# Optimization experiments

Hardware: AMD Instinct MI355X
Metric: run time of the kernel (lower is better)

Reference implementation:

```python
import jax, jax.numpy as jnp
import numpy as np
from jax import lax

BS, NT, CH, K = 8, 128, 1024, 4
H = 512  # num_output_chanls // 2 per direction (bidirectional)
G = 4 * H  # gate dim, PyTorch order i,f,g,o


def setup_inputs() -> dict:
    key = jax.random.key(0)
    ks = jax.random.split(key, 9)
    s = 1.0 / np.sqrt(H)
    u = lambda k_, shape: jax.random.uniform(k_, shape, jnp.float32, -s, s)
    return {
        "inputs": jax.random.normal(ks[0], (BS, NT, CH, K), jnp.float32),
        "Wih_f": u(ks[1], (K, G, CH)),
        "Whh_f": u(ks[2], (K, G, H)),
        "bih_f": u(ks[3], (K, G)),
        "bhh_f": u(ks[4], (K, G)),
        "Wih_b": u(ks[5], (K, G, CH)),
        "Whh_b": u(ks[6], (K, G, H)),
        "bih_b": u(ks[7], (K, G)),
        "bhh_b": u(ks[8], (K, G)),
    }


def _lstm_dir(x_tbck, Wih, Whh, bih, bhh, reverse):
    # x_tbck: [nt, bs, ch, k]; weights batched over k heads.
    bs = x_tbck.shape[1]
    k, _, h = Whh.shape
    bias = bih + bhh  # [k, 4h]

    def step(carry, x_t):
        h_prev, c_prev = carry
        # detach_hidden_state=True: hidden state detached each step
        h_prev = lax.stop_gradient(h_prev)
        c_prev = lax.stop_gradient(c_prev)
        gates = (jnp.einsum('bck,kgc->bkg', x_t, Wih)
                 + jnp.einsum('bkh,kgh->bkg', h_prev, Whh)
                 + bias)  # [bs, k, 4h]
        i, f, g, o = jnp.split(gates, 4, axis=-1)
        c_new = jax.nn.sigmoid(f) * c_prev + jax.nn.sigmoid(i) * jnp.tanh(g)
        h_new = jax.nn.sigmoid(o) * jnp.tanh(c_new)
        return (h_new, c_new), h_new

    init = (jnp.zeros((bs, k, h), x_tbck.dtype), jnp.zeros((bs, k, h), x_tbck.dtype))
    _, hs = lax.scan(step, init, x_tbck, reverse=reverse)  # [nt, bs, k, h]
    return hs


def reference(inputs, Wih_f, Whh_f, bih_f, bhh_f, Wih_b, Whh_b, bih_b, bhh_b):
    # inputs: [bs, nt, ch, k] -> scan over time
    x = jnp.transpose(inputs, (1, 0, 2, 3))  # [nt, bs, ch, k]
    hs_f = _lstm_dir(x, Wih_f, Whh_f, bih_f, bhh_f, reverse=False)
    hs_b = _lstm_dir(x, Wih_b, Whh_b, bih_b, bhh_b, reverse=True)
    # [nt, bs, k, h] -> [bs, nt, h, k]; concat forward/backward on hidden dim
    hs_f = jnp.transpose(hs_f, (1, 0, 3, 2))
    hs_b = jnp.transpose(hs_b, (1, 0, 3, 2))
    return jnp.concatenate([hs_f, hs_b], axis=2)  # [bs, nt, 2h, k]
```

## Files before the change

kernel.cpp:

```cpp
#include <hip/hip_runtime.h>
#include <stdint.h>


typedef __attribute__((ext_vector_type(8))) short short8;
typedef __attribute__((ext_vector_type(4))) float floatx4;
typedef unsigned long long ull;

#define POISON 0x7FC07FC07FC07FC0ull

#define GLOAD_LDS16(g, l)                                        \
  __builtin_amdgcn_global_load_lds(                              \
      (const __attribute__((address_space(1))) void*)(g),        \
      (__attribute__((address_space(3))) void*)(l), 16, 0, 0)

__device__ __forceinline__ unsigned short f2bf(float f) {
  unsigned u = __float_as_uint(f);
  u = (u + 0x7fffu + ((u >> 16) & 1u)) >> 16;
  return (unsigned short)u;
}
__device__ __forceinline__ float sigm(float x) { return 1.0f / (1.0f + __expf(-x)); }
__device__ __forceinline__ float tanh_f(float x) {
  float ax = fabsf(x);
  float e = __expf(-2.0f * ax);
  float t = (1.0f - e) / (1.0f + e);
  return x < 0.0f ? -t : t;
}

__global__ void pack_x_k(const float* __restrict__ x, unsigned short* __restrict__ Xp) {
  int g = blockIdx.x * 256 + threadIdx.x;
  int m = g >> 10, c = g & 1023;
  int t = m >> 3, b = m & 7;
  float4 v = *(const float4*)(x + ((size_t)((b * 128 + t) * 1024 + c)) * 4);
  Xp[g]           = f2bf(v.x);
  Xp[1048576 + g] = f2bf(v.y);
  Xp[2097152 + g] = f2bf(v.z);
  Xp[3145728 + g] = f2bf(v.w);
}

__global__ void cast_bf_k(const float* __restrict__ src, unsigned short* __restrict__ dst, int n4) {
  int i = blockIdx.x * 256 + threadIdx.x;
  if (i >= n4) return;
  float4 v = ((const float4*)src)[i];
  ushort4 o;
  o.x = f2bf(v.x); o.y = f2bf(v.y); o.z = f2bf(v.z); o.w = f2bf(v.w);
  ((ushort4*)dst)[i] = o;
}

__global__ void bias_k(const float* __restrict__ bihf, const float* __restrict__ bhhf,
                       const float* __restrict__ bihb, const float* __restrict__ bhhb,
                       float* __restrict__ bias) {
  int i = blockIdx.x * 256 + threadIdx.x;
  int dk = i >> 11, g = i & 2047, kk = dk & 3;
  const float* a = (dk < 4) ? bihf : bihb;
  const float* b = (dk < 4) ? bhhf : bhhb;
  bias[i] = a[kk * 2048 + g] + b[kk * 2048 + g];
}

__global__ void fill_poison_k(ull* __restrict__ p) {
  p[(size_t)blockIdx.x * 256 + threadIdx.x] = POISON;
}

__global__ __launch_bounds__(256) void gemm_ih_k(
    const unsigned short* __restrict__ Xp, const unsigned short* __restrict__ Wb,
    const float* __restrict__ bias, float* __restrict__ ih) {
  const int mt = blockIdx.x, ntl = blockIdx.y, dk = blockIdx.z;
  const int kh = dk & 3;
  const int tid = threadIdx.x;
  const int L = tid & 63, w = tid >> 6;
  const int wm = w & 1, wn = w >> 1;
  const int quad = L >> 4, lo = L & 15;

  __shared__ unsigned short As[128 * 32];
  __shared__ unsigned short Bs[128 * 32];

  const unsigned short* Ab = Xp + (size_t)kh * 1048576 + (size_t)mt * 128 * 1024;
  const unsigned short* Bb = Wb + (size_t)dk * 2097152 + (size_t)ntl * 128 * 1024;

  floatx4 acc[4][4] = {};

  for (int kc = 0; kc < 32; ++kc) {
#pragma unroll
    for (int q = 0; q < 2; ++q) {
      int c = q * 256 + w * 64 + L;
      int ldsb = (q * 256 + w * 64) * 8;
      GLOAD_LDS16(Ab + (size_t)(c >> 2) * 1024 + kc * 32 + (c & 3) * 8, As + ldsb);
      GLOAD_LDS16(Bb + (size_t)(c >> 2) * 1024 + kc * 32 + (c & 3) * 8, Bs + ldsb);
    }
    __syncthreads();
    short8 af[4], bf[4];
#pragma unroll
    for (int mi = 0; mi < 4; ++mi)
      af[mi] = *(const short8*)(As + (wm * 64 + mi * 16 + lo) * 32 + quad * 8);
#pragma unroll
    for (int ni = 0; ni < 4; ++ni)
      bf[ni] = *(const short8*)(Bs + (wn * 64 + ni * 16 + lo) * 32 + quad * 8);
#pragma unroll
    for (int mi = 0; mi < 4; ++mi)
#pragma unroll
      for (int ni = 0; ni < 4; ++ni)
        acc[mi][ni] = __builtin_amdgcn_mfma_f32_16x16x32_bf16(af[mi], bf[ni], acc[mi][ni], 0, 0, 0);
    __syncthreads();
  }

#pragma unroll
  for (int mi = 0; mi < 4; ++mi)
#pragma unroll
    for (int ni = 0; ni < 4; ++ni) {
      int g = ntl * 128 + wn * 64 + ni * 16 + lo;
      float bv = bias[dk * 2048 + g];
#pragma unroll
      for (int r = 0; r < 4; ++r) {
        int m = mt * 128 + wm * 64 + mi * 16 + quad * 4 + r;
        ih[((size_t)dk * 1024 + m) * 2048 + g] = acc[mi][ni][r] + bv;
      }
    }
}

__global__ __launch_bounds__(256) void lstm_rec_k(
    const float* __restrict__ ih, const unsigned short* __restrict__ whh,
    float* __restrict__ out, ull* __restrict__ stateS) {
  const int tid = threadIdx.x;
  const int L = tid & 63;
  const int w = tid >> 6;
  const int grp = blockIdx.x & 7;
  const int d = grp >> 2, kh = grp & 3;
  const int wg = blockIdx.x >> 3;
  const int j0 = wg * 32;
  const int quad = L >> 4, lo = L & 15;

  __shared__ unsigned short h_lds[16 * 520];
  __shared__ float gbuf[4][8][32];

  for (int i = tid; i < 16 * 520; i += 256) h_lds[i] = 0;

  short8 bfrag[2][16];
#pragma unroll
  for (int ni = 0; ni < 2; ++ni) {
    const unsigned short* wb =
        whh + ((size_t)grp * 2048 + (size_t)(w * 512 + j0 + ni * 16 + lo)) * 512 + quad * 8;
#pragma unroll
    for (int kk = 0; kk < 16; ++kk) bfrag[ni][kk] = *(const short8*)(wb + kk * 32);
  }

  const int pb = tid >> 5, pjj = tid & 31;
  float creg = 0.0f;

  float ihv[2][4];
  {
    int t0 = d ? 127 : 0;
#pragma unroll
    for (int ni = 0; ni < 2; ++ni) {
      const float* ihp =
          ih + ((size_t)grp * 1024 + (size_t)t0 * 8) * 2048 + (w * 512 + j0 + ni * 16 + lo);
#pragma unroll
      for (int r = 0; r < 4; ++r) {
        int b = quad * 4 + r;
        ihv[ni][r] = (b < 8) ? ihp[(size_t)b * 2048] : 0.0f;
      }
    }
  }

  const int srow = tid >> 5;
  const int scol = (tid & 31) * 16;

  for (int s = 0; s < 128; ++s) {
    const int t = d ? (127 - s) : s;

    if (s) {
      const ull* src = stateS + ((size_t)grp * 128 + s) * 1024 + tid * 4;
      ull v0, v1, v2, v3;
      do {
        v0 = __hip_atomic_load(src + 0, __ATOMIC_RELAXED, __HIP_MEMORY_SCOPE_AGENT);
        v1 = __hip_atomic_load(src + 1, __ATOMIC_RELAXED, __HIP_MEMORY_SCOPE_AGENT);
        v2 = __hip_atomic_load(src + 2, __ATOMIC_RELAXED, __HIP_MEMORY_SCOPE_AGENT);
        v3 = __hip_atomic_load(src + 3, __ATOMIC_RELAXED, __HIP_MEMORY_SCOPE_AGENT);
      } while (v0 == POISON || v1 == POISON || v2 == POISON || v3 == POISON);
      unsigned short* dl = h_lds + srow * 520 + scol;
      *(ull*)(dl + 0) = v0;
      *(ull*)(dl + 4) = v1;
      *(ull*)(dl + 8) = v2;
      *(ull*)(dl + 12) = v3;
    }
    __syncthreads();

    floatx4 acc[2] = {};
    {
      const unsigned short* ar = h_lds + lo * 520 + quad * 8;
#pragma unroll
      for (int kk = 0; kk < 16; ++kk) {
        short8 a = *(const short8*)(ar + kk * 32);
#pragma unroll
        for (int ni = 0; ni < 2; ++ni)
          acc[ni] = __builtin_amdgcn_mfma_f32_16x16x32_bf16(a, bfrag[ni][kk], acc[ni], 0, 0, 0);
      }
    }
#pragma unroll
    for (int ni = 0; ni < 2; ++ni)
#pragma unroll
      for (int r = 0; r < 4; ++r) {
        int b = quad * 4 + r;
        if (b < 8) gbuf[w][b][ni * 16 + lo] = acc[ni][r] + ihv[ni][r];
      }

    if (s < 127) {
      int tn = d ? (126 - s) : (s + 1);
#pragma unroll
      for (int ni = 0; ni < 2; ++ni) {
        const float* ihp =
            ih + ((size_t)grp * 1024 + (size_t)tn * 8) * 2048 + (w * 512 + j0 + ni * 16 + lo);
#pragma unroll
        for (int r = 0; r < 4; ++r) {
          int b = quad * 4 + r;
          ihv[ni][r] = (b < 8) ? ihp[(size_t)b * 2048] : 0.0f;
        }
      }
    }
    __syncthreads();

    {
      float ig = gbuf[0][pb][pjj], fg = gbuf[1][pb][pjj];
      float gg = gbuf[2][pb][pjj], og = gbuf[3][pb][pjj];
      float cn = sigm(fg) * creg + sigm(ig) * tanh_f(gg);
      creg = cn;
      float h = sigm(og) * tanh_f(cn);

      if (s < 127) {
        unsigned hs = f2bf(h);
        int base = L & ~3;
        unsigned v0 = __shfl(hs, base + 0);
        unsigned v1 = __shfl(hs, base + 1);
        unsigned v2 = __shfl(hs, base + 2);
        unsigned v3 = __shfl(hs, base + 3);
        if ((L & 3) == 0) {
          ull wv = (ull)v0 | ((ull)v1 << 16) | ((ull)v2 << 32) | ((ull)v3 << 48);
          ull* dst = stateS + ((size_t)grp * 128 + (s + 1)) * 1024 + pb * 128 + ((j0 + pjj) >> 2);
          __hip_atomic_store(dst, wv, __ATOMIC_RELAXED, __HIP_MEMORY_SCOPE_AGENT);
        }
      }
      out[(((size_t)pb * 128 + t) * 1024 + d * 512 + j0 + pjj) * 4 + kh] = h;
    }
  }
}

extern "C" void kernel_launch(void* const* d_in, const int* in_sizes, int n_in,
                              void* d_out, int out_size, void* d_ws, size_t ws_size,
                              hipStream_t stream) {
  (void)in_sizes; (void)n_in; (void)out_size; (void)ws_size;
  const float* x     = (const float*)d_in[0];
  const float* Wih_f = (const float*)d_in[1];
  const float* Whh_f = (const float*)d_in[2];
  const float* bih_f = (const float*)d_in[3];
  const float* bhh_f = (const float*)d_in[4];
  const float* Wih_b = (const float*)d_in[5];
  const float* Whh_b = (const float*)d_in[6];
  const float* bih_b = (const float*)d_in[7];
  const float* bhh_b = (const float*)d_in[8];
  float* out = (float*)d_out;
  char* ws = (char*)d_ws;

  float* bias          = (float*)(ws + (256u << 10));
  float* ihg           = (float*)(ws + (1ull << 20));
  unsigned short* Xp   = (unsigned short*)(ws + (65ull << 20));
  unsigned short* Wihb = (unsigned short*)(ws + (73ull << 20));
  unsigned short* Whhb = (unsigned short*)(ws + (65ull << 20));
  ull* stateS          = (ull*)(ws + (81ull << 20));

  pack_x_k<<<4096, 256, 0, stream>>>(x, Xp);
  cast_bf_k<<<8192, 256, 0, stream>>>(Wih_f, Wihb, 2097152);
  cast_bf_k<<<8192, 256, 0, stream>>>(Wih_b, Wihb + 8388608, 2097152);
  bias_k<<<64, 256, 0, stream>>>(bih_f, bhh_f, bih_b, bhh_b, bias);
  gemm_ih_k<<<dim3(8, 16, 8), 256, 0, stream>>>(Xp, Wihb, bias, ihg);
  cast_bf_k<<<4096, 256, 0, stream>>>(Whh_f, Whhb, 1048576);
  cast_bf_k<<<4096, 256, 0, stream>>>(Whh_b, Whhb + 4194304, 1048576);
  fill_poison_k<<<4096, 256, 0, stream>>>(stateS);
  lstm_rec_k<<<128, 256, 0, stream>>>(ihg, Whhb, out, stateS);
}
```

Before: 496.3 us.

## Fuse prep kernels and poll recurrent state with vectorized inline-asm loads

Merges the x packing, Wih casts and bias sums into one launch, and the Whh casts plus poison fill into a second, cutting launches from eight to four. In the recurrent kernel, polling on the cross-block hidden state now uses two 16-byte global loads with the sc0 cache bit in inline assembly, and falls back to the original 64-bit atomic loop after a bounded number of tries. The producer also writes the state with a volatile store before the atomic store. This aims to lower per-step handoff latency, at the cost of relying on the memory semantics of the hand-written loads and a redundant store.

```diff
diff --git a/kernel.cpp b/kernel.cpp
--- a/kernel.cpp
+++ b/kernel.cpp
@@ -4,9 +4,11 @@
 
 typedef __attribute__((ext_vector_type(8))) short short8;
 typedef __attribute__((ext_vector_type(4))) float floatx4;
+typedef __attribute__((ext_vector_type(4))) unsigned uintx4;
 typedef unsigned long long ull;
 
 #define POISON 0x7FC07FC07FC07FC0ull
+#define P32 0x7FC07FC0u
 
 #define GLOAD_LDS16(g, l)                                        \
   __builtin_amdgcn_global_load_lds(                              \
@@ -26,38 +28,54 @@
   return x < 0.0f ? -t : t;
 }
 
-__global__ void pack_x_k(const float* __restrict__ x, unsigned short* __restrict__ Xp) {
-  int g = blockIdx.x * 256 + threadIdx.x;
-  int m = g >> 10, c = g & 1023;
-  int t = m >> 3, b = m & 7;
-  float4 v = *(const float4*)(x + ((size_t)((b * 128 + t) * 1024 + c)) * 4);
-  Xp[g]           = f2bf(v.x);
-  Xp[1048576 + g] = f2bf(v.y);
-  Xp[2097152 + g] = f2bf(v.z);
-  Xp[3145728 + g] = f2bf(v.w);
-}
-
-__global__ void cast_bf_k(const float* __restrict__ src, unsigned short* __restrict__ dst, int n4) {
-  int i = blockIdx.x * 256 + threadIdx.x;
-  if (i >= n4) return;
+__device__ __forceinline__ void cast4(const float* __restrict__ src,
+                                      unsigned short* __restrict__ dst, int i) {
   float4 v = ((const float4*)src)[i];
   ushort4 o;
   o.x = f2bf(v.x); o.y = f2bf(v.y); o.z = f2bf(v.z); o.w = f2bf(v.w);
   ((ushort4*)dst)[i] = o;
 }
 
-__global__ void bias_k(const float* __restrict__ bihf, const float* __restrict__ bhhf,
-                       const float* __restrict__ bihb, const float* __restrict__ bhhb,
-                       float* __restrict__ bias) {
-  int i = blockIdx.x * 256 + threadIdx.x;
-  int dk = i >> 11, g = i & 2047, kk = dk & 3;
-  const float* a = (dk < 4) ? bihf : bihb;
-  const float* b = (dk < 4) ? bhhf : bhhb;
-  bias[i] = a[kk * 2048 + g] + b[kk * 2048 + g];
-}
-
-__global__ void fill_poison_k(ull* __restrict__ p) {
-  p[(size_t)blockIdx.x * 256 + threadIdx.x] = POISON;
+__global__ __launch_bounds__(256) void prep1_k(
+    const float* __restrict__ x, const float* __restrict__ WihF,
+    const float* __restrict__ WihB, const float* __restrict__ bihF,
+    const float* __restrict__ bhhF, const float* __restrict__ bihB,
+    const float* __restrict__ bhhB, unsigned short* __restrict__ Xp,
+    unsigned short* __restrict__ Wihb, float* __restrict__ bias) {
+  int blk = blockIdx.x, tid = threadIdx.x;
+  if (blk < 4096) {
+    int g = blk * 256 + tid;
+    int m = g >> 10, c = g & 1023;
+    int t = m >> 3, b = m & 7;
+    float4 v = *(const float4*)(x + ((size_t)((b * 128 + t) * 1024 + c)) * 4);
+    Xp[g]           = f2bf(v.x);
+    Xp[1048576 + g] = f2bf(v.y);
+    Xp[2097152 + g] = f2bf(v.z);
+    Xp[3145728 + g] = f2bf(v.w);
+  } else if (blk < 12288) {
+    cast4(WihF, Wihb, (blk - 4096) * 256 + tid);
+  } else if (blk < 20480) {
+    cast4(WihB, Wihb + 8388608, (blk - 12288) * 256 + tid);
+  } else {
+    int i = (blk - 20480) * 256 + tid;
+    int dk = i >> 11, g = i & 2047, kk = dk & 3;
+    const float* a = (dk < 4) ? bihF : bihB;
+    const float* b = (dk < 4) ? bhhF : bhhB;
+    bias[i] = a[kk * 2048 + g] + b[kk * 2048 + g];
+  }
+}
+
+__global__ __launch_bounds__(256) void prep2_k(
+    const float* __restrict__ WhhF, const float* __restrict__ WhhB,
+    unsigned short* __restrict__ Whhb, ull* __restrict__ stateS) {
+  int blk = blockIdx.x, tid = threadIdx.x;
+  if (blk < 4096) {
+    cast4(WhhF, Whhb, blk * 256 + tid);
+  } else if (blk < 8192) {
+    cast4(WhhB, Whhb + 4194304, (blk - 4096) * 256 + tid);
+  } else {
+    stateS[(size_t)(blk - 8192) * 256 + tid] = POISON;
+  }
 }
 
 __global__ __launch_bounds__(256) void gemm_ih_k(
@@ -168,18 +186,39 @@
 
     if (s) {
       const ull* src = stateS + ((size_t)grp * 128 + s) * 1024 + tid * 4;
-      ull v0, v1, v2, v3;
-      do {
-        v0 = __hip_atomic_load(src + 0, __ATOMIC_RELAXED, __HIP_MEMORY_SCOPE_AGENT);
-        v1 = __hip_atomic_load(src + 1, __ATOMIC_RELAXED, __HIP_MEMORY_SCOPE_AGENT);
-        v2 = __hip_atomic_load(src + 2, __ATOMIC_RELAXED, __HIP_MEMORY_SCOPE_AGENT);
-        v3 = __hip_atomic_load(src + 3, __ATOMIC_RELAXED, __HIP_MEMORY_SCOPE_AGENT);
-      } while (v0 == POISON || v1 == POISON || v2 == POISON || v3 == POISON);
       unsigned short* dl = h_lds + srow * 520 + scol;
-      *(ull*)(dl + 0) = v0;
-      *(ull*)(dl + 4) = v1;
-      *(ull*)(dl + 8) = v2;
-      *(ull*)(dl + 12) = v3;
+      uintx4 A, B;
+      bool ok = false;
+      for (int it = 0; it < 24; ++it) {
+        asm volatile(
+            "global_load_dwordx4 %0, %2, off sc0\n\t"
+            "global_load_dwordx4 %1, %2, off offset:16 sc0\n\t"
+            "s_waitcnt vmcnt(0)"
+            : "=&v"(A), "=&v"(B)
+            : "v"(src)
+            : "memory");
+        if (!(A[0] == P32 || A[1] == P32 || A[2] == P32 || A[3] == P32 ||
+              B[0] == P32 || B[1] == P32 || B[2] == P32 || B[3] == P32)) {
+          ok = true;
+          break;
+        }
+      }
+      if (ok) {
+        *(uintx4*)(dl) = A;
+        *(uintx4*)(dl + 8) = B;
+      } else {
+        ull v0, v1, v2, v3;
+        do {
+          v0 = __hip_atomic_load(src + 0, __ATOMIC_RELAXED, __HIP_MEMORY_SCOPE_AGENT);
+          v1 = __hip_atomic_load(src + 1, __ATOMIC_RELAXED, __HIP_MEMORY_SCOPE_AGENT);
+          v2 = __hip_atomic_load(src + 2, __ATOMIC_RELAXED, __HIP_MEMORY_SCOPE_AGENT);
+          v3 = __hip_atomic_load(src + 3, __ATOMIC_RELAXED, __HIP_MEMORY_SCOPE_AGENT);
+        } while (v0 == POISON || v1 == POISON || v2 == POISON || v3 == POISON);
+        *(ull*)(dl + 0) = v0;
+        *(ull*)(dl + 4) = v1;
+        *(ull*)(dl + 8) = v2;
+        *(ull*)(dl + 12) = v3;
+      }
     }
     __syncthreads();
 
@@ -234,7 +273,9 @@
         if ((L & 3) == 0) {
           ull wv = (ull)v0 | ((ull)v1 << 16) | ((ull)v2 << 32) | ((ull)v3 << 48);
           ull* dst = stateS + ((size_t)grp * 128 + (s + 1)) * 1024 + pb * 128 + ((j0 + pjj) >> 2);
-          __hip_atomic_store(dst, wv, __ATOMIC_RELAXED, __HIP_MEMORY_SCOPE_AGENT);
+          *(volatile ull*)dst = wv;
+          __hip_atomic_store(dst, wv, __ATOMIC_RELAXED,
+                             __HIP_MEMORY_SCOPE_AGENT);
         }
       }
       out[(((size_t)pb * 128 + t) * 1024 + d * 512 + j0 + pjj) * 4 + kh] = h;
@@ -265,13 +306,9 @@
   unsigned short* Whhb = (unsigned short*)(ws + (65ull << 20));
   ull* stateS          = (ull*)(ws + (81ull << 20));
 
-  pack_x_k<<<4096, 256, 0, stream>>>(x, Xp);
-  cast_bf_k<<<8192, 256, 0, stream>>>(Wih_f, Wihb, 2097152);
-  cast_bf_k<<<8192, 256, 0, stream>>>(Wih_b, Wihb + 8388608, 2097152);
-  bias_k<<<64, 256, 0, stream>>>(bih_f, bhh_f, bih_b, bhh_b, bias);
+  prep1_k<<<20544, 256, 0, stream>>>(x, Wih_f, Wih_b, bih_f, bhh_f, bih_b, bhh_b,
+                                     Xp, Wihb, bias);
   gemm_ih_k<<<dim3(8, 16, 8), 256, 0, stream>>>(Xp, Wihb, bias, ihg);
-  cast_bf_k<<<4096, 256, 0, stream>>>(Whh_f, Whhb, 1048576);
-  cast_bf_k<<<4096, 256, 0, stream>>>(Whh_b, Whhb + 4194304, 1048576);
-  fill_poison_k<<<4096, 256, 0, stream>>>(stateS);
+  prep2_k<<<12288, 256, 0, stream>>>(Whh_f, Whh_b, Whhb, stateS);
   lstm_rec_k<<<128, 256, 0, stream>>>(ihg, Whhb, out, stateS);
 }
```

Measured after the change: 873.3 us. +76.0%, slower.
